# Performance work log

Hardware: AMD Instinct MI355X
Metric: run time of the kernel (lower is better)

The kernel has to match this reference:

```python
import jax, jax.numpy as jnp
import numpy as np

N = 27          # n_agents
NA = 33         # n_actions
OFF = 6         # semantic_action_offset
ATK = NA - OFF  # 27 attack actions
HID = 256       # rnn_hidden_dim
HEADS = 4
HD = 16         # head_dim
V = 8           # comm_value_dim
REL = 5
TOPK = 4
IN = 322
FLAT = HEADS * V  # 32
FUSE_SCALE = 0.1
GATE_FLOOR = 0.0
NEG = -1e10


def setup_inputs() -> dict:
    key = jax.random.key(0)
    ks = iter(jax.random.split(key, 40))
    r = lambda *s: jax.random.normal(next(ks), s, dtype=jnp.float32) * 0.05
    BS = 1024
    inp = {
        'inputs': jax.random.normal(next(ks), (BS * N, IN), dtype=jnp.float32),
        'hidden_state': jax.random.normal(next(ks), (BS * N, HID), dtype=jnp.float32),
        'relation_features': jax.random.normal(next(ks), (BS, N, N, REL), dtype=jnp.float32),
        'W1': r(HID, IN), 'b1': r(HID),
        'Wih': r(3 * HID, HID), 'bih': r(3 * HID),
        'Whh': r(3 * HID, HID), 'bhh': r(3 * HID),
        'Wp1': r(HID, HID), 'bp1': r(HID),
        'Wp2': r(NA, HID), 'bp2': r(NA),
        'Wq': r(HEADS * HD, HID), 'bq': r(HEADS * HD),
        'Wk': r(HEADS * HD, HID + REL), 'bk': r(HEADS * HD),
        'Wv': r(HEADS * V, ATK + 2), 'bv': r(HEADS * V),
        'ln_g': jnp.ones((FLAT,), jnp.float32), 'ln_b': jnp.zeros((FLAT,), jnp.float32),
        'Wg1': r(HID, HID + FLAT), 'bg1': r(HID),
        'Wg2': r(1, HID), 'bg2': jnp.full((1,), -2.5, jnp.float32),  # attack_gate_init_bias
        'Wd1': r(HID, HID + FLAT), 'bd1': r(HID),
        'Wd2': r(ATK, HID) * 0.2, 'bd2': r(ATK) * 0.2,  # small random instead of zero-init for nontrivial test
        'null_key': r(HEADS, HD), 'null_value': r(HEADS, V),
        'bs': BS,
    }
    return inp


def _topk_mask(scores, k):
    # scores: [bs, N, N+1, HEADS]; keep top-k along axis 2
    st = jnp.moveaxis(scores, 2, -1)                # [bs, N, HEADS, N+1]
    thr = jax.lax.top_k(st, k)[0][..., -1:]
    st = jnp.where(st >= thr, st, NEG)
    return jnp.moveaxis(st, -1, 2)


def _forward(inputs, hidden_state, relation_features, W1, b1, Wih, bih, Whh, bhh,
             Wp1, bp1, Wp2, bp2, Wq, bq, Wk, bk, Wv, bv, ln_g, ln_b,
             Wg1, bg1, Wg2, bg2, Wd1, bd1, Wd2, bd2, null_key, null_value, bs):
    x = jax.nn.relu(inputs @ W1.T + b1)
    h_in = hidden_state.reshape(-1, HID)
    # PyTorch GRUCell
    gi = x @ Wih.T + bih
    gh = h_in @ Whh.T + bhh
    ir, iz, inn = jnp.split(gi, 3, axis=-1)
    hr, hz, hn = jnp.split(gh, 3, axis=-1)
    rg = jax.nn.sigmoid(ir + hr)
    zg = jax.nn.sigmoid(iz + hz)
    ng = jnp.tanh(inn + rg * hn)
    h = (1.0 - zg) * ng + zg * h_in

    ah = h.reshape(bs, N, HID)                       # agent_hidden
    logits = jax.nn.relu(ah @ Wp1.T + bp1) @ Wp2.T + bp2   # [bs,N,NA]
    base_logits = logits[:, :, :OFF]
    attack_logits = logits[:, :, OFF:]

    # intent features (avail_actions=None path)
    attack_probs = jax.nn.softmax(attack_logits, axis=-1)
    top1 = jnp.max(attack_probs, axis=-1, keepdims=True)
    can_attack = jnp.ones((bs, N, 1), attack_probs.dtype)
    value_source = jnp.concatenate([attack_probs, can_attack, top1], axis=-1)
    sender_values = (value_source @ Wv.T + bv).reshape(bs, N, HEADS, V)

    queries = (ah @ Wq.T + bq).reshape(bs, N, HEADS, HD)
    # Linear over concat([sender_hidden, relation]) == split-weight sum
    Wk_h, Wk_r = Wk[:, :HID], Wk[:, HID:]
    key_h = ah @ Wk_h.T                              # [bs, N(send), A]
    key_r = jnp.einsum('bijr,ar->bija', relation_features, Wk_r)
    pair_keys = (key_h[:, None, :, :] + key_r + bk).reshape(bs, N, N, HEADS, HD)

    scale = 1.0 / np.sqrt(HD)
    scores = jnp.einsum('bihd,bijhd->bijh', queries, pair_keys) * scale
    eye = jnp.eye(N, dtype=bool)[None, :, :, None]
    scores = jnp.where(eye, NEG, scores)
    null_scores = jnp.einsum('bihd,hd->bih', queries, null_key)[:, :, None, :] * scale
    scores = jnp.concatenate([scores, null_scores], axis=2)   # [bs,N,N+1,HEADS]

    alpha = jax.nn.softmax(_topk_mask(scores, TOPK), axis=2)
    messages = (jnp.einsum('bijh,bjhv->bihv', alpha[:, :, :N], sender_values)
                + alpha[:, :, N, :, None] * null_value)        # [bs,N,HEADS,V]
    flat = messages.reshape(bs, N, FLAT)
    mu = jnp.mean(flat, axis=-1, keepdims=True)
    var = jnp.var(flat, axis=-1, keepdims=True)
    normed = (flat - mu) * jax.lax.rsqrt(var + 1e-5) * ln_g + ln_b

    fusion = jnp.concatenate([ah, normed], axis=-1)
    raw_gate = jax.nn.sigmoid(jax.nn.relu(fusion @ Wg1.T + bg1) @ Wg2.T + bg2)
    gate = GATE_FLOOR + (1.0 - GATE_FLOOR) * raw_gate
    delta = jax.nn.relu(fusion @ Wd1.T + bd1) @ Wd2.T + bd2
    fused = attack_logits + FUSE_SCALE * gate * delta
    final = jnp.concatenate([base_logits, fused], axis=-1).reshape(bs * N, NA)
    return final, h


def reference(inputs, hidden_state, relation_features, W1, b1, Wih, bih, Whh, bhh,
              Wp1, bp1, Wp2, bp2, Wq, bq, Wk, bk, Wv, bv, ln_g, ln_b,
              Wg1, bg1, Wg2, bg2, Wd1, bd1, Wd2, bd2, null_key, null_value, bs):
    return _forward(inputs, hidden_state, relation_features, W1, b1, Wih, bih, Whh, bhh,
                    Wp1, bp1, Wp2, bp2, Wq, bq, Wk, bk, Wv, bv, ln_g, ln_b,
                    Wg1, bg1, Wg2, bg2, Wd1, bd1, Wd2, bd2, null_key, null_value, bs)
```

## Files before the change

### kernel.cpp

```cpp
#include <hip/hip_runtime.h>
#include <cstdint>
#include <cstddef>

#define ROWS 27648
#define NEGV (-1e10f)

typedef __attribute__((ext_vector_type(8))) short bf16x8;
typedef __attribute__((ext_vector_type(4))) short short4v;
typedef __attribute__((ext_vector_type(4))) float f32x4;

__device__ __forceinline__ float sigmoidf_(float x) { return 1.f / (1.f + __expf(-x)); }
__device__ __forceinline__ float bf2f(short s) {
  union { float f; unsigned u; } x; x.u = ((unsigned)(unsigned short)s) << 16; return x.f;
}
__device__ __forceinline__ short f2bf(float f) {
  union { float f; unsigned u; } x; x.f = f;
  unsigned r = (x.u + 0x7fffu + ((x.u >> 16) & 1u)) >> 16;
  return (short)r;
}

#define GLDS(gp, lp) __builtin_amdgcn_global_load_lds( \
  (const __attribute__((address_space(1))) void*)(gp), \
  (__attribute__((address_space(3))) void*)(lp), 16, 0, 0)

template <int ACT, int BF16OUT>
__global__ __launch_bounds__(256) void gemm_mfma(
    const short* __restrict__ A, int lda,
    const short* __restrict__ B, int ldb,
    const float* __restrict__ bias,
    void* __restrict__ Cv, int ldc, int nstore, int K) {
  __shared__ short As[128 * 32];
  __shared__ short Bs[128 * 32];
  const int tid = threadIdx.x;
  const int wave = tid >> 6, lane = tid & 63;
  const int m0 = blockIdx.x * 128, n0 = blockIdx.y * 128;
  const int srow = lane >> 2, scol = (lane & 3) * 8;
  const int sr0 = wave * 32;
  const int wm = (wave >> 1) * 64, wn = (wave & 1) * 64;
  const int fr = lane & 15, fk = (lane >> 4) * 8;

  f32x4 acc[4][4] = {};

  const short* pA0 = A + (size_t)(m0 + sr0 + srow) * lda + scol;
  const short* pA1 = pA0 + 16 * lda;
  const short* pB0 = B + (size_t)(n0 + sr0 + srow) * ldb + scol;
  const short* pB1 = pB0 + 16 * ldb;
  short* lA0 = &As[sr0 * 32];
  short* lA1 = &As[(sr0 + 16) * 32];
  short* lB0 = &Bs[sr0 * 32];
  short* lB1 = &Bs[(sr0 + 16) * 32];

  for (int k0 = 0; k0 < K; k0 += 32) {
    GLDS(pA0 + k0, lA0);
    GLDS(pA1 + k0, lA1);
    GLDS(pB0 + k0, lB0);
    GLDS(pB1 + k0, lB1);
    __syncthreads();
    bf16x8 af[4], bfr[4];
#pragma unroll
    for (int t = 0; t < 4; ++t) {
      af[t]  = *(const bf16x8*)&As[(wm + t * 16 + fr) * 32 + fk];
      bfr[t] = *(const bf16x8*)&Bs[(wn + t * 16 + fr) * 32 + fk];
    }
#pragma unroll
    for (int i = 0; i < 4; ++i)
#pragma unroll
      for (int j = 0; j < 4; ++j)
        acc[i][j] = __builtin_amdgcn_mfma_f32_16x16x32_bf16(af[i], bfr[j], acc[i][j], 0, 0, 0);
    __syncthreads();
  }

  const int rbase = m0 + wm + (lane >> 4) * 4;
#pragma unroll
  for (int j = 0; j < 4; ++j) {
    const int col = n0 + wn + j * 16 + fr;
    if (col >= nstore) continue;
    const float bv = bias ? bias[col] : 0.f;
#pragma unroll
    for (int i = 0; i < 4; ++i)
#pragma unroll
      for (int r = 0; r < 4; ++r) {
        const int row = rbase + i * 16 + r;
        float v = acc[i][j][r] + bv;
        if (ACT) v = fmaxf(v, 0.f);
        if (BF16OUT) ((short*)Cv)[(size_t)row * ldc + col] = f2bf(v);
        else         ((float*)Cv)[(size_t)row * ldc + col] = v;
      }
  }
}

__global__ __launch_bounds__(256) void gemm_pqk(
    const short* __restrict__ A, const short* __restrict__ B,
    const float* __restrict__ bias,
    short* __restrict__ P1, float* __restrict__ QK) {
  __shared__ short As[128 * 32];
  __shared__ short Bs[128 * 32];
  const int tid = threadIdx.x;
  const int wave = tid >> 6, lane = tid & 63;
  const int m0 = blockIdx.x * 128, n0 = blockIdx.y * 128;
  const int srow = lane >> 2, scol = (lane & 3) * 8;
  const int sr0 = wave * 32;
  const int wm = (wave >> 1) * 64, wn = (wave & 1) * 64;
  const int fr = lane & 15, fk = (lane >> 4) * 8;

  f32x4 acc[4][4] = {};
  const short* pA0 = A + (size_t)(m0 + sr0 + srow) * 288 + scol;
  const short* pA1 = pA0 + 16 * 288;
  const short* pB0 = B + (size_t)(n0 + sr0 + srow) * 256 + scol;
  const short* pB1 = pB0 + 16 * 256;
  short* lA0 = &As[sr0 * 32];
  short* lA1 = &As[(sr0 + 16) * 32];
  short* lB0 = &Bs[sr0 * 32];
  short* lB1 = &Bs[(sr0 + 16) * 32];

  for (int k0 = 0; k0 < 256; k0 += 32) {
    GLDS(pA0 + k0, lA0);
    GLDS(pA1 + k0, lA1);
    GLDS(pB0 + k0, lB0);
    GLDS(pB1 + k0, lB1);
    __syncthreads();
    bf16x8 af[4], bfr[4];
#pragma unroll
    for (int t = 0; t < 4; ++t) {
      af[t]  = *(const bf16x8*)&As[(wm + t * 16 + fr) * 32 + fk];
      bfr[t] = *(const bf16x8*)&Bs[(wn + t * 16 + fr) * 32 + fk];
    }
#pragma unroll
    for (int i = 0; i < 4; ++i)
#pragma unroll
      for (int j = 0; j < 4; ++j)
        acc[i][j] = __builtin_amdgcn_mfma_f32_16x16x32_bf16(af[i], bfr[j], acc[i][j], 0, 0, 0);
    __syncthreads();
  }

  const int rbase = m0 + wm + (lane >> 4) * 4;
#pragma unroll
  for (int j = 0; j < 4; ++j) {
    const int col = n0 + wn + j * 16 + fr;
    if (col >= 384) continue;
    const float bv = bias[col];
#pragma unroll
    for (int i = 0; i < 4; ++i)
#pragma unroll
      for (int r = 0; r < 4; ++r) {
        const int row = rbase + i * 16 + r;
        float v = acc[i][j][r] + bv;
        if (col < 256) {
          P1[(size_t)row * 256 + col] = f2bf(fmaxf(v, 0.f));
        } else {
          QK[(size_t)row * 128 + (col - 256)] = v;
        }
      }
  }
}

__global__ __launch_bounds__(256) void conv_all(
    const float* __restrict__ inputs, const float* __restrict__ hidden,
    const float* __restrict__ W1, const float* __restrict__ Wih,
    const float* __restrict__ Whh, const float* __restrict__ Wp1,
    const float* __restrict__ Wp2, const float* __restrict__ Wq,
    const float* __restrict__ Wk, const float* __restrict__ Wg1,
    const float* __restrict__ Wd1, const float* __restrict__ Wg2,
    const float* __restrict__ Wd2, const float* __restrict__ bp1,
    const float* __restrict__ bq, const float* __restrict__ bg1,
    const float* __restrict__ bd1, const float* __restrict__ bg2,
    const float* __restrict__ bd2,
    short* __restrict__ xin, short* __restrict__ hid,
    short* __restrict__ w1w, short* __restrict__ wihw, short* __restrict__ whhw,
    short* __restrict__ wp2w, short* __restrict__ wpqk, short* __restrict__ wgdw,
    short* __restrict__ wfw, float* __restrict__ bpqkb, float* __restrict__ bgd,
    float* __restrict__ bf2v) {
  const int NX = ROWS * 352;
  const int NH = ROWS * 256;
  int idx = blockIdx.x * 256 + threadIdx.x;
  if (idx < NX) {
    int row = idx / 352, c = idx - row * 352;
    xin[idx] = (c < 322) ? f2bf(inputs[row * 322 + c]) : (short)0;
    return;
  }
  idx -= NX;
  if (idx < NH) { hid[idx] = f2bf(hidden[idx]); return; }
  idx -= NH;
  if (idx < 90112) {
    int r = idx / 352, c = idx - r * 352;
    w1w[idx] = (c < 322) ? f2bf(W1[r * 322 + c]) : (short)0;
    return;
  }
  idx -= 90112;
  if (idx < 196608) { wihw[idx] = f2bf(Wih[idx]); return; }
  idx -= 196608;
  if (idx < 196608) { whhw[idx] = f2bf(Whh[idx]); return; }
  idx -= 196608;
  if (idx < 32768) {
    wp2w[idx] = (idx < 33 * 256) ? f2bf(Wp2[idx]) : (short)0;
    return;
  }
  idx -= 32768;
  if (idx < 131072) {
    int r = idx >> 8, c = idx & 255;
    short v = 0;
    if (r < 256) v = f2bf(Wp1[r * 256 + c]);
    else if (r < 320) v = f2bf(Wq[(r - 256) * 256 + c]);
    else if (r < 384) v = f2bf(Wk[(size_t)(r - 320) * 261 + c]);
    wpqk[idx] = v;
    return;
  }
  idx -= 131072;
  if (idx < 147456) {
    wgdw[idx] = (idx < 73728) ? f2bf(Wg1[idx]) : f2bf(Wd1[idx - 73728]);
    return;
  }
  idx -= 147456;
  if (idx < 65536) {
    int r = idx >> 9, c = idx & 511;
    short v = 0;
    if (r == 0 && c < 256) v = f2bf(Wg2[c]);
    else if (r >= 1 && r < 28 && c >= 256) v = f2bf(Wd2[(r - 1) * 256 + (c - 256)]);
    wfw[idx] = v;
    return;
  }
  idx -= 65536;
  if (idx < 384) {
    bpqkb[idx] = (idx < 256) ? bp1[idx] : ((idx < 320) ? bq[idx - 256] : 0.f);
    return;
  }
  idx -= 384;
  if (idx < 512) { bgd[idx] = (idx < 256) ? bg1[idx] : bd1[idx - 256]; return; }
  idx -= 512;
  if (idx < 128)
    bf2v[idx] = (idx == 0) ? bg2[0] : ((idx < 28) ? bd2[idx - 1] : 0.f);
}

__global__ __launch_bounds__(256) void gru_kernel(
    const short* __restrict__ GI, const short* __restrict__ GH,
    const float* __restrict__ Hin, float* __restrict__ H,
    short* __restrict__ FUS) {
  int idx = blockIdx.x * 256 + threadIdx.x;
  int row = idx >> 6;
  int c = (idx & 63) * 4;
  const short4v gr = *(const short4v*)(GI + (size_t)row * 768 + c);
  const short4v gz = *(const short4v*)(GI + (size_t)row * 768 + 256 + c);
  const short4v gn = *(const short4v*)(GI + (size_t)row * 768 + 512 + c);
  const short4v hr = *(const short4v*)(GH + (size_t)row * 768 + c);
  const short4v hz = *(const short4v*)(GH + (size_t)row * 768 + 256 + c);
  const short4v hn = *(const short4v*)(GH + (size_t)row * 768 + 512 + c);
  const f32x4 hi = *(const f32x4*)(Hin + (size_t)row * 256 + c);
  f32x4 o;
  short4v ob;
#pragma unroll
  for (int p = 0; p < 4; ++p) {
    float r = sigmoidf_(bf2f(gr[p]) + bf2f(hr[p]));
    float z = sigmoidf_(bf2f(gz[p]) + bf2f(hz[p]));
    float n = tanhf(bf2f(gn[p]) + r * bf2f(hn[p]));
    float h = (1.f - z) * n + z * hi[p];
    o[p] = h;
    ob[p] = f2bf(h);
  }
  *(f32x4*)(H + (size_t)row * 256 + c) = o;
  *(short4v*)(FUS + (size_t)row * 288 + c) = ob;
}

__global__ __launch_bounds__(256) void sv_kernel(
    const float* __restrict__ logits, const float* __restrict__ Wv,
    const float* __restrict__ bv, float* __restrict__ SV) {
  const int wave = threadIdx.x >> 6;
  const int lane = threadIdx.x & 63;
  const int row = blockIdx.x * 4 + wave;
  __shared__ float vs_s[4][29];
  float v = (lane < 27) ? logits[(size_t)row * 33 + 6 + lane] : -INFINITY;
  float m = v;
#pragma unroll
  for (int off = 32; off; off >>= 1) m = fmaxf(m, __shfl_xor(m, off));
  float e = (lane < 27) ? __expf(v - m) : 0.f;
  float s = e;
#pragma unroll
  for (int off = 32; off; off >>= 1) s += __shfl_xor(s, off);
  if (lane < 27) vs_s[wave][lane] = e / s;
  if (lane == 27) vs_s[wave][27] = 1.f;
  if (lane == 28) vs_s[wave][28] = 1.f / s;
  __syncthreads();
  if (lane < 32) {
    float acc = bv[lane];
    const float* w = Wv + lane * 29;
#pragma unroll
    for (int c = 0; c < 29; ++c) acc += w[c] * vs_s[wave][c];
    SV[(size_t)row * 32 + lane] = acc;
  }
}

__global__ __launch_bounds__(256) void attn4_kernel(
    const float* __restrict__ QK, const float* __restrict__ rel,
    const float* __restrict__ Wk, const float* __restrict__ bk,
    const float* __restrict__ SV, const float* __restrict__ null_key,
    const float* __restrict__ null_value, const float* __restrict__ ln_g,
    const float* __restrict__ ln_b, short* __restrict__ FUS) {
  const int b  = blockIdx.x;
  const int iq = blockIdx.y;
  const int t = threadIdx.x;
  const int wave = t >> 6, lane = t & 63;
  const int i = iq * 4 + wave;
  const int iw = (i < 27) ? i : 26;

  __shared__ float kh_s[64 * 29];
  __shared__ float sv_s[28 * 32];
  __shared__ float q_s[4][64];
  __shared__ float wkr_s[320];
  __shared__ float bk_s[64], nk_s[64];
  __shared__ float lng_s[32], lnb_s[32];
  __shared__ float rel_s[4][136];
  __shared__ float qws[4][28];
  __shared__ float s_row[4][112];

  for (int idx = t; idx < 27 * 64; idx += 256) {
    int r = idx >> 6, c = idx & 63;
    kh_s[c * 29 + r] = QK[(size_t)(b * 27 + r) * 128 + 64 + c];
  }
  for (int idx = t; idx < 27 * 32; idx += 256)
    sv_s[idx] = SV[(size_t)b * 864 + idx];
  q_s[wave][lane] = QK[(size_t)(b * 27 + iw) * 128 + lane];
  for (int idx = t; idx < 320; idx += 256) {
    int a = idx / 5, r = idx - a * 5;
    wkr_s[idx] = Wk[(size_t)a * 261 + 256 + r];
  }
  if (t < 64) bk_s[t] = bk[t];
  else if (t < 128) nk_s[t - 64] = null_key[t - 64];
  else if (t < 160) sv_s[27 * 32 + (t - 128)] = null_value[t - 128];
  else if (t < 192) { lng_s[t - 160] = ln_g[t - 160]; lnb_s[t - 160] = ln_b[t - 160]; }
  for (int idx = lane; idx < 135; idx += 64)
    rel_s[wave][idx] = rel[(size_t)(b * 27 + iw) * 135 + idx];
  __syncthreads();

  if (lane < 28) {
    float acc = 0.f;
    if (lane < 20) {
      const int h = lane / 5, r = lane - h * 5;
#pragma unroll
      for (int d = 0; d < 16; ++d)
        acc += q_s[wave][h * 16 + d] * wkr_s[(h * 16 + d) * 5 + r];
    } else if (lane < 24) {
      const int h = lane - 20;
#pragma unroll
      for (int d = 0; d < 16; ++d)
        acc += q_s[wave][h * 16 + d] * bk_s[h * 16 + d];
    } else {
      const int h = lane - 24;
#pragma unroll
      for (int d = 0; d < 16; ++d)
        acc += q_s[wave][h * 16 + d] * nk_s[h * 16 + d];
    }
    qws[wave][lane] = acc;
  }
  __builtin_amdgcn_wave_barrier();

#pragma unroll
  for (int pass = 0; pass < 2; ++pass) {
    const int item = pass * 64 + lane;
    if (item < 112) {
      const int j = item >> 2, h = item & 3;
      float s;
      if (j < 27) {
        float acc = qws[wave][20 + h];
        const float* q  = &q_s[wave][h * 16];
        const float* kh = &kh_s[(h * 16) * 29 + j];
#pragma unroll
        for (int d = 0; d < 16; ++d) acc += q[d] * kh[d * 29];
        const float* rp = &rel_s[wave][j * 5];
        const float* qw = &qws[wave][h * 5];
#pragma unroll
        for (int r = 0; r < 5; ++r) acc += rp[r] * qw[r];
        s = acc * 0.25f;
        if (j == i) s = NEGV;
      } else {
        s = qws[wave][24 + h] * 0.25f;
      }
      s_row[wave][item] = s;
    }
  }
  __builtin_amdgcn_wave_barrier();

  {
    const int g = lane >> 4;
    const int li = lane & 15;
    const int j1 = li + 16;
    const float v0 = s_row[wave][li * 4 + g];
    const float v1 = (j1 < 28) ? s_row[wave][j1 * 4 + g] : -INFINITY;
    float w0 = v0, w1 = v1;
    float m0 = 0.f, thr = 0.f;
#pragma unroll
    for (int r = 0; r < 4; ++r) {
      float gm = fmaxf(w0, w1);
#pragma unroll
      for (int off = 8; off; off >>= 1) gm = fmaxf(gm, __shfl_xor(gm, off));
      if (r == 0) m0 = gm;
      thr = gm;
      const unsigned long long b0 = __ballot(w0 == gm);
      const unsigned long long b1 = __ballot(w1 == gm);
      const unsigned seg0 = (unsigned)(b0 >> (g * 16)) & 0xFFFFu;
      const unsigned seg1 = (unsigned)(b1 >> (g * 16)) & 0xFFFFu;
      if (seg0) { if (li == __builtin_ctz(seg0)) w0 = -INFINITY; }
      else      { if (li == __builtin_ctz(seg1)) w1 = -INFINITY; }
    }
    float e0 = (v0 >= thr) ? __expf(v0 - m0) : 0.f;
    float e1 = (j1 < 28 && v1 >= thr) ? __expf(v1 - m0) : 0.f;
    float s = e0 + e1;
#pragma unroll
    for (int off = 8; off; off >>= 1) s += __shfl_xor(s, off);
    const float inv = 1.f / s;
    s_row[wave][li * 4 + g] = e0 * inv;
    if (j1 < 28) s_row[wave][j1 * 4 + g] = e1 * inv;
  }
  __builtin_amdgcn_wave_barrier();

  {
    const int sl = lane & 31;
    const int h = sl >> 3;
    const int jbase = (lane >> 5) * 14;
    const float* al = &s_row[wave][h];
    float acc = 0.f;
#pragma unroll
    for (int jj = 0; jj < 14; ++jj)
      acc += al[(jbase + jj) * 4] * sv_s[(jbase + jj) * 32 + sl];
    acc += __shfl_xor(acc, 32);
    float sum = acc;
#pragma unroll
    for (int off = 16; off; off >>= 1) sum += __shfl_xor(sum, off);
    const float mu = sum * (1.f / 32.f);
    const float d = acc - mu;
    float sq = d * d;
#pragma unroll
    for (int off = 16; off; off >>= 1) sq += __shfl_xor(sq, off);
    const float rs = rsqrtf(sq * (1.f / 32.f) + 1e-5f);
    const float nv = d * rs * lng_s[sl] + lnb_s[sl];
    if (i < 27 && lane < 32)
      FUS[(size_t)(b * 27 + i) * 288 + 256 + sl] = f2bf(nv);
  }
}

__global__ __launch_bounds__(256) void fuse_kernel(
    const float* __restrict__ GDf, const float* __restrict__ LOG,
    float* __restrict__ out) {
  int idx = blockIdx.x * 256 + threadIdx.x;
  int row = idx / 33, c = idx - row * 33;
  float v = LOG[idx];
  if (c >= 6) {
    float gate = sigmoidf_(GDf[(size_t)row * 28]);
    v += 0.1f * gate * GDf[(size_t)row * 28 + (c - 5)];
  }
  out[idx] = v;
}

extern "C" void kernel_launch(void* const* d_in, const int* in_sizes, int n_in,
                              void* d_out, int out_size, void* d_ws, size_t ws_size,
                              hipStream_t stream) {
  const float* inputs = (const float*)d_in[0];
  const float* hidden = (const float*)d_in[1];
  const float* rel    = (const float*)d_in[2];
  const float* W1  = (const float*)d_in[3];  const float* b1  = (const float*)d_in[4];
  const float* Wih = (const float*)d_in[5];  const float* bih = (const float*)d_in[6];
  const float* Whh = (const float*)d_in[7];  const float* bhh = (const float*)d_in[8];
  const float* Wp1 = (const float*)d_in[9];  const float* bp1 = (const float*)d_in[10];
  const float* Wp2 = (const float*)d_in[11]; const float* bp2 = (const float*)d_in[12];
  const float* Wq  = (const float*)d_in[13]; const float* bq  = (const float*)d_in[14];
  const float* Wk  = (const float*)d_in[15]; const float* bk  = (const float*)d_in[16];
  const float* Wv  = (const float*)d_in[17]; const float* bv  = (const float*)d_in[18];
  const float* ln_g = (const float*)d_in[19]; const float* ln_b = (const float*)d_in[20];
  const float* Wg1 = (const float*)d_in[21]; const float* bg1 = (const float*)d_in[22];
  const float* Wg2 = (const float*)d_in[23]; const float* bg2 = (const float*)d_in[24];
  const float* Wd1 = (const float*)d_in[25]; const float* bd1 = (const float*)d_in[26];
  const float* Wd2 = (const float*)d_in[27]; const float* bd2 = (const float*)d_in[28];
  const float* null_key   = (const float*)d_in[29];
  const float* null_value = (const float*)d_in[30];

  char* wsb = (char*)d_ws;
  short* GIB = (short*)(wsb + 0);
  short* GDB = (short*)(wsb + 0);
  short* XINB = (short*)(wsb + 42467328);
  short* GHB  = (short*)(wsb + 42467328);
  float* LOG  = (float*)(wsb + 42467328);
  float* QKB  = (float*)(wsb + 42467328 + 4194304);
  float* SVB  = (float*)(wsb + 42467328 + 18874368);
  float* LOGD = (float*)(wsb + 42467328 + 23068672);
  short* XB   = (short*)(wsb + 84934656);
  short* FUS  = (short*)(wsb + 84934656);
  short* HIDB = (short*)(wsb + 84934656 + 16777216);
  short* P1B  = (short*)(wsb + 84934656 + 16777216);
  char* wb = wsb + 115867648;
  short* W1W   = (short*)(wb + 0);
  short* WIHW  = (short*)(wb + 180224);
  short* WHHW  = (short*)(wb + 573440);
  short* WP2W  = (short*)(wb + 966656);
  short* WPQK  = (short*)(wb + 1032192);
  short* WGDW  = (short*)(wb + 1294336);
  short* WFW   = (short*)(wb + 1589248);
  float* BPQKb = (float*)(wb + 1720320);
  float* BGD   = (float*)(wb + 1721856);
  float* BF2   = (float*)(wb + 1723904);

  float* out = (float*)d_out;
  float* H   = out + (size_t)ROWS * 33;

  conv_all<<<69028, 256, 0, stream>>>(inputs, hidden,
                                      W1, Wih, Whh, Wp1, Wp2, Wq, Wk, Wg1, Wd1,
                                      Wg2, Wd2, bp1, bq, bg1, bd1, bg2, bd2,
                                      XINB, HIDB,
                                      W1W, WIHW, WHHW, WP2W, WPQK, WGDW, WFW,
                                      BPQKb, BGD, BF2);
  gemm_mfma<1, 1><<<dim3(216, 2), 256, 0, stream>>>(XINB, 352, W1W, 352, b1, XB, 256, 256, 352);
  gemm_mfma<0, 1><<<dim3(216, 6), 256, 0, stream>>>(XB, 256, WIHW, 256, bih, GIB, 768, 768, 256);
  gemm_mfma<0, 1><<<dim3(216, 6), 256, 0, stream>>>(HIDB, 256, WHHW, 256, bhh, GHB, 768, 768, 256);
  gru_kernel<<<6912, 256, 0, stream>>>(GIB, GHB, hidden, H, FUS);
  gemm_pqk<<<dim3(216, 3), 256, 0, stream>>>(FUS, WPQK, BPQKb, P1B, QKB);
  gemm_mfma<0, 0><<<dim3(216, 1), 256, 0, stream>>>(P1B, 256, WP2W, 256, bp2, LOG, 33, 33, 256);
  sv_kernel<<<6912, 256, 0, stream>>>(LOG, Wv, bv, SVB);
  attn4_kernel<<<dim3(1024, 7), 256, 0, stream>>>(QKB, rel, Wk, bk, SVB, null_key,
                                                  null_value, ln_g, ln_b, FUS);
  gemm_mfma<1, 1><<<dim3(216, 4), 256, 0, stream>>>(FUS, 288, WGDW, 288, BGD, GDB, 512, 512, 288);
  gemm_mfma<0, 0><<<dim3(216, 1), 256, 0, stream>>>(GDB, 512, WFW, 512, BF2, LOGD, 28, 28, 512);
  fuse_kernel<<<3564, 256, 0, stream>>>(LOGD, LOG, out);
}
```

Baseline: 415.8 us.

## Widen GEMM K-tile to 64 with XOR-swizzled LDS layout

The MFMA GEMM kernels now stage 64-wide K slices per iteration instead of 32. Each slice is stored in shared memory with an XOR swizzle on the column chunk, which halves the number of barrier pairs per K and is meant to avoid LDS bank conflicts on the fragment reads. A tail path covers K values that are not a multiple of 64 (352, 288) with a separate 32-wide buffer. Shared memory is now dynamic, 32–48 KB per block instead of 16 KB, which may reduce occupancy.

```diff
diff --git a/kernel.cpp b/kernel.cpp
--- a/kernel.cpp
+++ b/kernel.cpp
@@ -29,45 +29,74 @@
     const short* __restrict__ B, int ldb,
     const float* __restrict__ bias,
     void* __restrict__ Cv, int ldc, int nstore, int K) {
-  __shared__ short As[128 * 32];
-  __shared__ short Bs[128 * 32];
+  extern __shared__ short smem[];
+  short* As = smem;
+  short* Bs = smem + 8192;
   const int tid = threadIdx.x;
   const int wave = tid >> 6, lane = tid & 63;
   const int m0 = blockIdx.x * 128, n0 = blockIdx.y * 128;
-  const int srow = lane >> 2, scol = (lane & 3) * 8;
+  const int srow = lane >> 3;
+  const int scol = ((lane & 7) ^ srow) * 8;
   const int sr0 = wave * 32;
   const int wm = (wave >> 1) * 64, wn = (wave & 1) * 64;
   const int fr = lane & 15, fk = (lane >> 4) * 8;
 
   f32x4 acc[4][4] = {};
 
-  const short* pA0 = A + (size_t)(m0 + sr0 + srow) * lda + scol;
-  const short* pA1 = pA0 + 16 * lda;
-  const short* pB0 = B + (size_t)(n0 + sr0 + srow) * ldb + scol;
-  const short* pB1 = pB0 + 16 * ldb;
-  short* lA0 = &As[sr0 * 32];
-  short* lA1 = &As[(sr0 + 16) * 32];
-  short* lB0 = &Bs[sr0 * 32];
-  short* lB1 = &Bs[(sr0 + 16) * 32];
-
-  for (int k0 = 0; k0 < K; k0 += 32) {
-    GLDS(pA0 + k0, lA0);
-    GLDS(pA1 + k0, lA1);
-    GLDS(pB0 + k0, lB0);
-    GLDS(pB1 + k0, lB1);
+  const short* pA = A + (size_t)(m0 + sr0 + srow) * lda + scol;
+  const short* pB = B + (size_t)(n0 + sr0 + srow) * ldb + scol;
+  short* lA = &As[sr0 * 64];
+  short* lB = &Bs[sr0 * 64];
+
+  const int KB = K & ~63;
+  for (int k0 = 0; k0 < KB; k0 += 64) {
+#pragma unroll
+    for (int g = 0; g < 4; ++g) {
+      GLDS(pA + k0 + g * 8 * lda, lA + g * 512);
+      GLDS(pB + k0 + g * 8 * ldb, lB + g * 512);
+    }
+    __syncthreads();
+#pragma unroll
+    for (int ks = 0; ks < 2; ++ks) {
+      bf16x8 af[4], bfr[4];
+#pragma unroll
+      for (int t = 0; t < 4; ++t) {
+        const int ra = wm + t * 16 + fr;
+        const int rb = wn + t * 16 + fr;
+        af[t]  = *(const bf16x8*)&As[(ra * 64 + ks * 32 + fk) ^ ((ra & 7) << 3)];
+        bfr[t] = *(const bf16x8*)&Bs[(rb * 64 + ks * 32 + fk) ^ ((rb & 7) << 3)];
+      }
+#pragma unroll
+      for (int i = 0; i < 4; ++i)
+#pragma unroll
+        for (int j = 0; j < 4; ++j)
+          acc[i][j] = __builtin_amdgcn_mfma_f32_16x16x32_bf16(af[i], bfr[j], acc[i][j], 0, 0, 0);
+    }
+    __syncthreads();
+  }
+
+  if (K & 32) {
+    short* As2 = smem + 16384;
+    short* Bs2 = smem + 20480;
+    const int sr2 = lane >> 2, sc2 = (lane & 3) * 8;
+    const short* qA = A + (size_t)(m0 + sr0 + sr2) * lda + sc2 + KB;
+    const short* qB = B + (size_t)(n0 + sr0 + sr2) * ldb + sc2 + KB;
+    GLDS(qA, &As2[sr0 * 32]);
+    GLDS(qA + 16 * lda, &As2[(sr0 + 16) * 32]);
+    GLDS(qB, &Bs2[sr0 * 32]);
+    GLDS(qB + 16 * ldb, &Bs2[(sr0 + 16) * 32]);
     __syncthreads();
     bf16x8 af[4], bfr[4];
 #pragma unroll
     for (int t = 0; t < 4; ++t) {
-      af[t]  = *(const bf16x8*)&As[(wm + t * 16 + fr) * 32 + fk];
-      bfr[t] = *(const bf16x8*)&Bs[(wn + t * 16 + fr) * 32 + fk];
+      af[t]  = *(const bf16x8*)&As2[(wm + t * 16 + fr) * 32 + fk];
+      bfr[t] = *(const bf16x8*)&Bs2[(wn + t * 16 + fr) * 32 + fk];
     }
 #pragma unroll
     for (int i = 0; i < 4; ++i)
 #pragma unroll
       for (int j = 0; j < 4; ++j)
         acc[i][j] = __builtin_amdgcn_mfma_f32_16x16x32_bf16(af[i], bfr[j], acc[i][j], 0, 0, 0);
-    __syncthreads();
   }
 
   const int rbase = m0 + wm + (lane >> 4) * 4;
@@ -93,43 +122,47 @@
     const short* __restrict__ A, const short* __restrict__ B,
     const float* __restrict__ bias,
     short* __restrict__ P1, float* __restrict__ QK) {
-  __shared__ short As[128 * 32];
-  __shared__ short Bs[128 * 32];
+  extern __shared__ short smem[];
+  short* As = smem;
+  short* Bs = smem + 8192;
   const int tid = threadIdx.x;
   const int wave = tid >> 6, lane = tid & 63;
   const int m0 = blockIdx.x * 128, n0 = blockIdx.y * 128;
-  const int srow = lane >> 2, scol = (lane & 3) * 8;
+  const int srow = lane >> 3;
+  const int scol = ((lane & 7) ^ srow) * 8;
   const int sr0 = wave * 32;
   const int wm = (wave >> 1) * 64, wn = (wave & 1) * 64;
   const int fr = lane & 15, fk = (lane >> 4) * 8;
 
   f32x4 acc[4][4] = {};
-  const short* pA0 = A + (size_t)(m0 + sr0 + srow) * 288 + scol;
-  const short* pA1 = pA0 + 16 * 288;
-  const short* pB0 = B + (size_t)(n0 + sr0 + srow) * 256 + scol;
-  const short* pB1 = pB0 + 16 * 256;
-  short* lA0 = &As[sr0 * 32];
-  short* lA1 = &As[(sr0 + 16) * 32];
-  short* lB0 = &Bs[sr0 * 32];
-  short* lB1 = &Bs[(sr0 + 16) * 32];
-
-  for (int k0 = 0; k0 < 256; k0 += 32) {
-    GLDS(pA0 + k0, lA0);
-    GLDS(pA1 + k0, lA1);
-    GLDS(pB0 + k0, lB0);
-    GLDS(pB1 + k0, lB1);
+  const short* pA = A + (size_t)(m0 + sr0 + srow) * 288 + scol;
+  const short* pB = B + (size_t)(n0 + sr0 + srow) * 256 + scol;
+  short* lA = &As[sr0 * 64];
+  short* lB = &Bs[sr0 * 64];
+
+  for (int k0 = 0; k0 < 256; k0 += 64) {
+#pragma unroll
+    for (int g = 0; g < 4; ++g) {
+      GLDS(pA + k0 + g * 8 * 288, lA + g * 512);
+      GLDS(pB + k0 + g * 8 * 256, lB + g * 512);
+    }
     __syncthreads();
-    bf16x8 af[4], bfr[4];
-#pragma unroll
-    for (int t = 0; t < 4; ++t) {
-      af[t]  = *(const bf16x8*)&As[(wm + t * 16 + fr) * 32 + fk];
-      bfr[t] = *(const bf16x8*)&Bs[(wn + t * 16 + fr) * 32 + fk];
-    }
-#pragma unroll
-    for (int i = 0; i < 4; ++i)
-#pragma unroll
-      for (int j = 0; j < 4; ++j)
-        acc[i][j] = __builtin_amdgcn_mfma_f32_16x16x32_bf16(af[i], bfr[j], acc[i][j], 0, 0, 0);
+#pragma unroll
+    for (int ks = 0; ks < 2; ++ks) {
+      bf16x8 af[4], bfr[4];
+#pragma unroll
+      for (int t = 0; t < 4; ++t) {
+        const int ra = wm + t * 16 + fr;
+        const int rb = wn + t * 16 + fr;
+        af[t]  = *(const bf16x8*)&As[(ra * 64 + ks * 32 + fk) ^ ((ra & 7) << 3)];
+        bfr[t] = *(const bf16x8*)&Bs[(rb * 64 + ks * 32 + fk) ^ ((rb & 7) << 3)];
+      }
+#pragma unroll
+      for (int i = 0; i < 4; ++i)
+#pragma unroll
+        for (int j = 0; j < 4; ++j)
+          acc[i][j] = __builtin_amdgcn_mfma_f32_16x16x32_bf16(af[i], bfr[j], acc[i][j], 0, 0, 0);
+    }
     __syncthreads();
   }
 
@@ -505,16 +538,16 @@
                                       XINB, HIDB,
                                       W1W, WIHW, WHHW, WP2W, WPQK, WGDW, WFW,
                                       BPQKb, BGD, BF2);
-  gemm_mfma<1, 1><<<dim3(216, 2), 256, 0, stream>>>(XINB, 352, W1W, 352, b1, XB, 256, 256, 352);
-  gemm_mfma<0, 1><<<dim3(216, 6), 256, 0, stream>>>(XB, 256, WIHW, 256, bih, GIB, 768, 768, 256);
-  gemm_mfma<0, 1><<<dim3(216, 6), 256, 0, stream>>>(HIDB, 256, WHHW, 256, bhh, GHB, 768, 768, 256);
+  gemm_mfma<1, 1><<<dim3(216, 2), 256, 49152, stream>>>(XINB, 352, W1W, 352, b1, XB, 256, 256, 352);
+  gemm_mfma<0, 1><<<dim3(216, 6), 256, 32768, stream>>>(XB, 256, WIHW, 256, bih, GIB, 768, 768, 256);
+  gemm_mfma<0, 1><<<dim3(216, 6), 256, 32768, stream>>>(HIDB, 256, WHHW, 256, bhh, GHB, 768, 768, 256);
   gru_kernel<<<6912, 256, 0, stream>>>(GIB, GHB, hidden, H, FUS);
-  gemm_pqk<<<dim3(216, 3), 256, 0, stream>>>(FUS, WPQK, BPQKb, P1B, QKB);
-  gemm_mfma<0, 0><<<dim3(216, 1), 256, 0, stream>>>(P1B, 256, WP2W, 256, bp2, LOG, 33, 33, 256);
+  gemm_pqk<<<dim3(216, 3), 256, 32768, stream>>>(FUS, WPQK, BPQKb, P1B, QKB);
+  gemm_mfma<0, 0><<<dim3(216, 1), 256, 32768, stream>>>(P1B, 256, WP2W, 256, bp2, LOG, 33, 33, 256);
   sv_kernel<<<6912, 256, 0, stream>>>(LOG, Wv, bv, SVB);
   attn4_kernel<<<dim3(1024, 7), 256, 0, stream>>>(QKB, rel, Wk, bk, SVB, null_key,
                                                   null_value, ln_g, ln_b, FUS);
-  gemm_mfma<1, 1><<<dim3(216, 4), 256, 0, stream>>>(FUS, 288, WGDW, 288, BGD, GDB, 512, 512, 288);
-  gemm_mfma<0, 0><<<dim3(216, 1), 256, 0, stream>>>(GDB, 512, WFW, 512, BF2, LOGD, 28, 28, 512);
+  gemm_mfma<1, 1><<<dim3(216, 4), 256, 49152, stream>>>(FUS, 288, WGDW, 288, BGD, GDB, 512, 512, 288);
+  gemm_mfma<0, 0><<<dim3(216, 1), 256, 32768, stream>>>(GDB, 512, WFW, 512, BF2, LOGD, 28, 28, 512);
   fuse_kernel<<<3564, 256, 0, stream>>>(LOGD, LOG, out);
 }
```

Result: faster. 404.5 us (-2.7%).
